# Kernel optimization log

Hardware: AMD Instinct MI355X
Metric: run time of the kernel (lower is better)

## Reference

```python
import math
import jax, jax.numpy as jnp
import numpy as np

B, T, D, H = 1, 4096, 1024, 16
HD = D // H  # 64

def setup_inputs() -> dict:
    key = jax.random.key(0)
    k1, k2, k3 = jax.random.split(key, 3)
    x = jax.random.normal(k1, (B, T, D), dtype=jnp.float32)
    # torch nn.Linear weight layout: [out_features, in_features]
    w_attn = jax.random.normal(k2, (3 * D, D), dtype=jnp.float32) * (1.0 / math.sqrt(D))
    w_proj = jax.random.normal(k3, (D, D), dtype=jnp.float32) * (1.0 / math.sqrt(D))
    return {"x": x, "w_attn": w_attn, "w_proj": w_proj}

def reference(x, w_attn, w_proj):
    b, t, d = x.shape
    qkv = jnp.einsum('btd,ed->bte', x, w_attn)  # [B,T,3D]
    q, k, v = jnp.split(qkv, 3, axis=-1)
    # [B,H,T,HD]
    q = q.reshape(b, t, H, HD).transpose(0, 2, 1, 3)
    k = k.reshape(b, t, H, HD).transpose(0, 2, 1, 3)
    v = v.reshape(b, t, H, HD).transpose(0, 2, 1, 3)
    scale = 1.0 / math.sqrt(HD)
    att = jnp.einsum('bhqd,bhkd->bhqk', q, k) * scale  # [B,H,T,T]
    causal = jnp.tril(jnp.ones((t, t), dtype=bool))
    att = jnp.where(causal[None, None], att, -jnp.inf)
    att = jax.nn.softmax(att, axis=-1)
    y = jnp.einsum('bhqk,bhkd->bhqd', att, v)  # [B,H,T,HD]
    y = y.transpose(0, 2, 1, 3).reshape(b, t, d)
    return jnp.einsum('btd,ed->bte', y, w_proj)
```

## Files before the change

### kernel.cpp

```cpp
#include <hip/hip_runtime.h>
#include <hip/hip_bf16.h>

typedef __bf16 bf16x8 __attribute__((ext_vector_type(8)));
typedef float  f32x4  __attribute__((ext_vector_type(4)));
typedef short  sh4    __attribute__((ext_vector_type(4)));

__device__ __forceinline__ void async_load16(const void* g, void* l) {
    __builtin_amdgcn_global_load_lds(
        (const __attribute__((address_space(1))) unsigned int*)g,
        (__attribute__((address_space(3))) unsigned int*)l,
        16, 0, 0);
}

__device__ __forceinline__ bool sniff_is_bf16(const void* src) {
    const unsigned int* p = (const unsigned int*)src;
    unsigned v = p[threadIdx.x & 63];
    unsigned e = (v >> 7) & 0xFF;
    unsigned long long m = __ballot(e >= 100 && e <= 140);
    return __popcll(m) >= 48;
}

__global__ __launch_bounds__(256) void to_bf16_3(
    const void* __restrict__ s0, const void* __restrict__ s1,
    const void* __restrict__ s2, __bf16* __restrict__ dst0) {
    const int b = blockIdx.x;
    const void* src; __bf16* dst; int boff;
    if (b < 4096)      { src = s0; dst = dst0;           boff = b; }
    else if (b < 7168) { src = s1; dst = dst0 + 4194304; boff = b - 4096; }
    else               { src = s2; dst = dst0 + 7340032; boff = b - 7168; }
    bool b16 = sniff_is_bf16(src);
    int i = boff * 1024 + threadIdx.x * 4;
    if (b16) {
        *(uint2*)(dst + i) = *(const uint2*)((const __bf16*)src + i);
    } else {
        float4 v = *(const float4*)((const float*)src + i);
        dst[i]     = (__bf16)v.x;
        dst[i + 1] = (__bf16)v.y;
        dst[i + 2] = (__bf16)v.z;
        dst[i + 3] = (__bf16)v.w;
    }
}

__global__ __launch_bounds__(256) void gemm_bt(
    const __bf16* __restrict__ A,
    const __bf16* __restrict__ B,
    __bf16* __restrict__ C,
    int M, int N, int K, int ldc,
    __bf16* __restrict__ vTout)
{
    __shared__ __bf16 As[3 * 128 * 32];
    __shared__ __bf16 Bs[3 * 128 * 32];

    const int nwg = gridDim.x;
    const int cpx = nwg >> 3;
    const int sid = (blockIdx.x & 7) * cpx + (blockIdx.x >> 3);
    const int nbx = N >> 7;
    const int bx  = sid % nbx;
    const int by  = sid / nbx;

    const int tid  = threadIdx.x;
    const int lane = tid & 63;
    const int w    = tid >> 6;
    const int wm   = w >> 1, wn = w & 1;
    const int m0   = by * 128;
    const int n0   = bx * 128;
    const int c    = lane & 15;
    const int g    = lane >> 4;

    f32x4 acc[4][4] = {};

    const int e0 = tid * 8;
    const int e1 = e0 + 2048;
    const int r0 = e0 >> 5, c0 = e0 & 31;
    const int r1 = e1 >> 5, c1 = e1 & 31;

    const __bf16* a0 = A + (size_t)(m0 + r0) * K + c0;
    const __bf16* a1 = A + (size_t)(m0 + r1) * K + c1;
    const __bf16* b0 = B + (size_t)(n0 + r0) * K + c0;
    const __bf16* b1 = B + (size_t)(n0 + r1) * K + c1;

    const int KT = K >> 5;

    async_load16(a0, As + e0);
    async_load16(a1, As + e1);
    async_load16(b0, Bs + e0);
    async_load16(b1, Bs + e1);
    async_load16(a0 + 32, As + 4096 + e0);
    async_load16(a1 + 32, As + 4096 + e1);
    async_load16(b0 + 32, Bs + 4096 + e0);
    async_load16(b1 + 32, Bs + 4096 + e1);

    int cb = 0, sb = 2;
    for (int kt = 0; kt < KT; ++kt) {
        if (kt + 1 < KT) asm volatile("s_waitcnt vmcnt(4)" ::: "memory");
        else             asm volatile("s_waitcnt vmcnt(0)" ::: "memory");
        __builtin_amdgcn_s_barrier();
        asm volatile("" ::: "memory");

        if (kt + 2 < KT) {
            const int k0 = (kt + 2) << 5;
            async_load16(a0 + k0, As + sb * 4096 + e0);
            async_load16(a1 + k0, As + sb * 4096 + e1);
            async_load16(b0 + k0, Bs + sb * 4096 + e0);
            async_load16(b1 + k0, Bs + sb * 4096 + e1);
        }

        const __bf16* as_ = As + cb * 4096;
        const __bf16* bs_ = Bs + cb * 4096;

        bf16x8 af[4], bfr[4];
        #pragma unroll
        for (int i = 0; i < 4; i++)
            af[i] = *(const bf16x8*)&as_[(wm * 64 + i * 16 + c) * 32 + g * 8];
        #pragma unroll
        for (int j = 0; j < 4; j++)
            bfr[j] = *(const bf16x8*)&bs_[(wn * 64 + j * 16 + c) * 32 + g * 8];
        #pragma unroll
        for (int i = 0; i < 4; i++)
            #pragma unroll
            for (int j = 0; j < 4; j++)
                acc[i][j] = __builtin_amdgcn_mfma_f32_16x16x32_bf16(af[i], bfr[j], acc[i][j], 0, 0, 0);

        cb = (cb == 2) ? 0 : cb + 1;
        sb = (sb == 2) ? 0 : sb + 1;
    }

    if (vTout && n0 >= ldc) {
        const int h0 = (n0 - ldc) >> 6;
        __bf16* Lt = As;
        __syncthreads();
        #pragma unroll
        for (int p = 0; p < 2; p++) {
            if (wn == p) {
                #pragma unroll
                for (int i = 0; i < 4; i++)
                    #pragma unroll
                    for (int j = 0; j < 4; j++) {
                        __bf16 tb[4] __attribute__((aligned(8)));
                        #pragma unroll
                        for (int r = 0; r < 4; r++) tb[r] = (__bf16)acc[i][j][r];
                        *(uint2*)&Lt[(j * 16 + c) * 136 + wm * 64 + i * 16 + g * 4]
                            = *(const uint2*)tb;
                    }
            }
            __syncthreads();
            {
                const int dl = tid >> 2, t0 = (tid & 3) * 32;
                __bf16* dst = vTout + (size_t)(h0 + p) * 262144 + (size_t)dl * 4096 + m0 + t0;
                #pragma unroll
                for (int k = 0; k < 4; k++)
                    *(bf16x8*)(dst + k * 8) = *(const bf16x8*)&Lt[dl * 136 + t0 + k * 8];
            }
            __syncthreads();
        }
        return;
    }

    #pragma unroll
    for (int i = 0; i < 4; i++) {
        const int row0 = m0 + wm * 64 + i * 16 + g * 4;
        #pragma unroll
        for (int j = 0; j < 4; j++) {
            const int col = n0 + wn * 64 + j * 16 + c;
            #pragma unroll
            for (int r = 0; r < 4; r++) {
                const size_t idx = (size_t)(row0 + r) * ldc + col;
                C[idx] = (__bf16)acc[i][j][r];
            }
        }
    }
}

__global__ __launch_bounds__(256) void gemm_bt64(
    const __bf16* __restrict__ A,
    const __bf16* __restrict__ B,
    void* __restrict__ Cv,
    int M, int N, int K,
    const void* sniff)
{
    bool out_b16 = true;
    if (sniff) out_b16 = sniff_is_bf16(sniff);

    __shared__ __bf16 As[3 * 128 * 32];
    __shared__ __bf16 Bs[3 * 64 * 32];

    const int nwg = gridDim.x;
    const int cpx = nwg >> 3;
    const int sid = (blockIdx.x & 7) * cpx + (blockIdx.x >> 3);
    const int nbx = N >> 6;
    const int bx  = sid % nbx;
    const int by  = sid / nbx;

    const int tid  = threadIdx.x;
    const int lane = tid & 63;
    const int w    = tid >> 6;
    const int wm   = w >> 1, wn = w & 1;
    const int m0   = by * 128;
    const int n0   = bx * 64;
    const int c    = lane & 15;
    const int g    = lane >> 4;

    f32x4 acc[4][2] = {};

    const int e0 = tid * 8;
    const int e1 = e0 + 2048;
    const int r0 = e0 >> 5, c0 = e0 & 31;
    const int r1 = e1 >> 5, c1 = e1 & 31;
    const int rb = tid >> 2, cbk = (tid & 3) * 8;

    const __bf16* a0 = A + (size_t)(m0 + r0) * K + c0;
    const __bf16* a1 = A + (size_t)(m0 + r1) * K + c1;
    const __bf16* bp = B + (size_t)(n0 + rb) * K + cbk;

    const int KT = K >> 5;

    async_load16(a0, As + e0);
    async_load16(a1, As + e1);
    async_load16(bp, Bs + e0);
    async_load16(a0 + 32, As + 4096 + e0);
    async_load16(a1 + 32, As + 4096 + e1);
    async_load16(bp + 32, Bs + 2048 + e0);

    int cb = 0, sb = 2;
    for (int kt = 0; kt < KT; ++kt) {
        if (kt + 1 < KT) asm volatile("s_waitcnt vmcnt(3)" ::: "memory");
        else             asm volatile("s_waitcnt vmcnt(0)" ::: "memory");
        __builtin_amdgcn_s_barrier();
        asm volatile("" ::: "memory");

        if (kt + 2 < KT) {
            const int k0 = (kt + 2) << 5;
            async_load16(a0 + k0, As + sb * 4096 + e0);
            async_load16(a1 + k0, As + sb * 4096 + e1);
            async_load16(bp + k0, Bs + sb * 2048 + e0);
        }

        const __bf16* as_ = As + cb * 4096;
        const __bf16* bs_ = Bs + cb * 2048;

        bf16x8 af[4], bfr[2];
        #pragma unroll
        for (int i = 0; i < 4; i++)
            af[i] = *(const bf16x8*)&as_[(wm * 64 + i * 16 + c) * 32 + g * 8];
        #pragma unroll
        for (int j = 0; j < 2; j++)
            bfr[j] = *(const bf16x8*)&bs_[(wn * 32 + j * 16 + c) * 32 + g * 8];
        #pragma unroll
        for (int i = 0; i < 4; i++)
            #pragma unroll
            for (int j = 0; j < 2; j++)
                acc[i][j] = __builtin_amdgcn_mfma_f32_16x16x32_bf16(af[i], bfr[j], acc[i][j], 0, 0, 0);

        cb = (cb == 2) ? 0 : cb + 1;
        sb = (sb == 2) ? 0 : sb + 1;
    }

    #pragma unroll
    for (int i = 0; i < 4; i++) {
        const int row0 = m0 + wm * 64 + i * 16 + g * 4;
        #pragma unroll
        for (int j = 0; j < 2; j++) {
            const int col = n0 + wn * 32 + j * 16 + c;
            #pragma unroll
            for (int r = 0; r < 4; r++) {
                const size_t idx = (size_t)(row0 + r) * N + col;
                if (out_b16) ((__bf16*)Cv)[idx] = (__bf16)acc[i][j][r];
                else         ((float*)Cv)[idx]  = acc[i][j][r];
            }
        }
    }
}

__global__ __launch_bounds__(512, 4) void attn_fwd(
    const __bf16* __restrict__ qkv,
    const __bf16* __restrict__ vT,
    __bf16* __restrict__ y)
{
    constexpr int LDQ = 2048;
    constexpr float SCL = 0.18033688011112042f;

    __shared__ __align__(16) char raw[50176];
    __bf16* ksb = (__bf16*)raw;
    __bf16* vsb = (__bf16*)(raw + 24576);
    float*  ls  = (float*)(raw + 49152);
    float*  F   = (float*)raw;

    const int id   = blockIdx.x;
    const int h    = (id & 7) * 2 + (id >> 8);
    const int pr   = (id >> 3) & 31;
    const int tid  = threadIdx.x;
    const int lane = tid & 63;
    const int w    = tid >> 6;
    const int kw   = w & 3;
    const int qw   = w >> 2;
    const int c    = lane & 15;
    const int g    = lane >> 4;
    const int qoff = h * 64;

    const int sr = tid >> 3, sg = ((tid & 7) ^ (sr & 7)) * 8;
    const __bf16* vbase = vT + (size_t)h * 262144;

    sh4 ones;
    #pragma unroll
    for (int i = 0; i < 4; i++) ones[i] = (short)0x3F80;

    const int qts[2] = {63 - pr, pr};

    #pragma unroll 1
    for (int ph = 0; ph < 2; ph++) {
        const int qt  = qts[ph];
        const int qs  = qt * 64;
        const int nkt = qt + 1;

        __syncthreads();

        async_load16(qkv + (size_t)sr * LDQ + 1024 + qoff + sg, ksb + tid * 8);
        async_load16(vbase + (size_t)sr * 4096 + sg, vsb + tid * 8);
        if (nkt > 1) {
            async_load16(qkv + (size_t)(64 + sr) * LDQ + 1024 + qoff + sg, ksb + 4096 + tid * 8);
            async_load16(vbase + (size_t)sr * 4096 + 64 + sg, vsb + 4096 + tid * 8);
        }

        bf16x8 qf[2][2];
        #pragma unroll
        for (int n = 0; n < 2; n++) {
            const __bf16* qrow = qkv + (size_t)(qs + qw * 32 + n * 16 + c) * LDQ + qoff;
            bf16x8 q0 = *(const bf16x8*)(qrow + g * 8);
            bf16x8 q1 = *(const bf16x8*)(qrow + 32 + g * 8);
            #pragma unroll
            for (int i = 0; i < 8; i++) {
                qf[n][0][i] = (__bf16)((float)q0[i] * SCL);
                qf[n][1][i] = (__bf16)((float)q1[i] * SCL);
            }
        }

        f32x4 ol[2] = {};
        f32x4 o[4][2] = {};

        for (int t = 0; t < nkt; t++) {
            if (t + 1 < nkt) asm volatile("s_waitcnt vmcnt(2)" ::: "memory");
            else             asm volatile("s_waitcnt vmcnt(0)" ::: "memory");
            __builtin_amdgcn_s_barrier();
            asm volatile("" ::: "memory");

            if (t + 2 < nkt) {
                const int nks = (t + 2) * 64;
                const int nb  = (t + 2) % 3;
                async_load16(qkv + (size_t)(nks + sr) * LDQ + 1024 + qoff + sg, ksb + (nb * 4096 + tid * 8));
                async_load16(vbase + (size_t)sr * 4096 + nks + sg, vsb + (nb * 4096 + tid * 8));
            }

            const __bf16* ks_ = ksb + (t % 3) * 4096;
            const __bf16* vs_ = vsb + (t % 3) * 4096;

            f32x4 sa[2] = {};
            #pragma unroll
            for (int s = 0; s < 2; s++) {
                bf16x8 kf = *(const bf16x8*)&ks_[(kw * 16 + c) * 64 + ((s * 4 + g) ^ (c & 7)) * 8];
                #pragma unroll
                for (int n = 0; n < 2; n++)
                    sa[n] = __builtin_amdgcn_mfma_f32_16x16x32_bf16(kf, qf[n][s], sa[n], 0, 0, 0);
            }

            if (t == nkt - 1) {
                #pragma unroll
                for (int n = 0; n < 2; n++)
                    #pragma unroll
                    for (int r = 0; r < 4; r++)
                        if (kw * 16 + g * 4 + r > qw * 32 + n * 16 + c) sa[n][r] = -1e30f;
            }

            sh4 vf[4];
            #pragma unroll
            for (int j = 0; j < 4; j++)
                vf[j] = *(const sh4*)&vs_[(j * 16 + c) * 64 + ((2 * kw + (g >> 1)) ^ (c & 7)) * 8 + (g & 1) * 4];

            #pragma unroll
            for (int n = 0; n < 2; n++) {
                __bf16 pb[4] __attribute__((aligned(8)));
                #pragma unroll
                for (int r = 0; r < 4; r++)
                    pb[r] = (__bf16)__builtin_amdgcn_exp2f(sa[n][r]);
                sh4 pbs = *(const sh4*)pb;
                ol[n] = __builtin_amdgcn_mfma_f32_16x16x16bf16_1k(ones, pbs, ol[n], 0, 0, 0);
                #pragma unroll
                for (int j = 0; j < 4; j++)
                    o[j][n] = __builtin_amdgcn_mfma_f32_16x16x16bf16_1k(vf[j], pbs, o[j][n], 0, 0, 0);
            }
        }

        __syncthreads();
        if (g == 0) {
            #pragma unroll
            for (int n = 0; n < 2; n++) ls[(kw * 4 + qw * 2 + n) * 16 + c] = ol[n][0];
        }
        __syncthreads();
        float rl = 0.f;
        if (w < 4) {
            float l_run = ls[(0 * 4 + w) * 16 + c] + ls[(1 * 4 + w) * 16 + c]
                        + ls[(2 * 4 + w) * 16 + c] + ls[(3 * 4 + w) * 16 + c];
            rl = 1.0f / l_run;
        }

        #pragma unroll
        for (int j = 0; j < 4; j++) {
            __syncthreads();
            #pragma unroll
            for (int n = 0; n < 2; n++)
                *(f32x4*)&F[((kw * 64) + (qw * 32 + n * 16 + c)) * 20 + g * 4] = o[j][n];
            __syncthreads();
            if (w < 4) {
                f32x4 t0 = *(const f32x4*)&F[((0 * 64) + (w * 16 + c)) * 20 + g * 4];
                f32x4 t1 = *(const f32x4*)&F[((1 * 64) + (w * 16 + c)) * 20 + g * 4];
                f32x4 t2 = *(const f32x4*)&F[((2 * 64) + (w * 16 + c)) * 20 + g * 4];
                f32x4 t3 = *(const f32x4*)&F[((3 * 64) + (w * 16 + c)) * 20 + g * 4];
                f32x4 tt = t0 + t1 + t2 + t3;
                __bf16 ob[4] __attribute__((aligned(8)));
                #pragma unroll
                for (int r = 0; r < 4; r++) ob[r] = (__bf16)(tt[r] * rl);
                *(uint2*)&y[(size_t)(qs + w * 16 + c) * 1024 + qoff + j * 16 + g * 4]
                    = *(const uint2*)ob;
            }
        }
    }
}

extern "C" void kernel_launch(void* const* d_in, const int* in_sizes, int n_in,
                              void* d_out, int out_size, void* d_ws, size_t ws_size,
                              hipStream_t stream) {
    constexpr int T = 4096, D = 1024;

    __bf16* cx   = (__bf16*)d_ws;
    __bf16* cwa  = cx  + (size_t)T * D;
    __bf16* cwp  = cwa + (size_t)3 * D * D;
    __bf16* qkv  = cwp + (size_t)D * D;
    __bf16* vT   = qkv + (size_t)T * 2048;
    __bf16* y    = vT  + (size_t)16 * 64 * T;

    to_bf16_3<<<8192, 256, 0, stream>>>(d_in[0], d_in[1], d_in[2], cx);
    gemm_bt<<<(3 * D / 128) * (T / 128), 256, 0, stream>>>(cx, cwa, qkv, T, 3 * D, D, 2048, vT);
    attn_fwd<<<512, 512, 0, stream>>>(qkv, vT, y);
    gemm_bt64<<<(D / 64) * (T / 128), 256, 0, stream>>>(y, cwp, d_out, T, D, D, d_in[2]);
}
```

Measured before the change: 190.1 us.

## Widen attention KV tile to 128 keys with double buffering

The attention kernel now processes 128 keys per iteration instead of 64. Each wave handles two 16-key sub-blocks, and the K/V LDS staging moves from a triple-buffered 64-key scheme to a double-buffered 128-key scheme. This halves the number of loop iterations and barriers and gives more MFMA work per sync. In exchange, LDS use rises to about 65KB, which may lower occupancy. Prefetch depth drops to one tile ahead and every iteration waits on vmcnt(0), so load latency may be less well hidden. The causal mask now works on absolute positions so it can handle a diagonal tile that falls partway through the 128-key tile.

Measured after the change: 192.3 us. About the same (+1.1%).

```diff
diff --git a/kernel.cpp b/kernel.cpp
--- a/kernel.cpp
+++ b/kernel.cpp
@@ -279,10 +279,10 @@
     constexpr int LDQ = 2048;
     constexpr float SCL = 0.18033688011112042f;
 
-    __shared__ __align__(16) char raw[50176];
+    __shared__ __align__(16) char raw[66560];
     __bf16* ksb = (__bf16*)raw;
-    __bf16* vsb = (__bf16*)(raw + 24576);
-    float*  ls  = (float*)(raw + 49152);
+    __bf16* vsb = (__bf16*)(raw + 32768);
+    float*  ls  = (float*)(raw + 65536);
     float*  F   = (float*)raw;
 
     const int id   = blockIdx.x;
@@ -297,7 +297,11 @@
     const int g    = lane >> 4;
     const int qoff = h * 64;
 
-    const int sr = tid >> 3, sg = ((tid & 7) ^ (sr & 7)) * 8;
+    const int p1  = tid + 512;
+    const int kr0 = tid >> 3, kc0 = ((tid & 7) ^ (kr0 & 7)) * 8;
+    const int kr1 = p1 >> 3,  kc1 = ((p1 & 7) ^ (kr1 & 7)) * 8;
+    const int dr0 = tid >> 4, vc0 = ((tid & 15) ^ (dr0 & 7)) * 8;
+    const int dr1 = p1 >> 4,  vc1 = ((p1 & 15) ^ (dr1 & 7)) * 8;
     const __bf16* vbase = vT + (size_t)h * 262144;
 
     sh4 ones;
@@ -310,16 +314,14 @@
     for (int ph = 0; ph < 2; ph++) {
         const int qt  = qts[ph];
         const int qs  = qt * 64;
-        const int nkt = qt + 1;
+        const int nkt = (qt >> 1) + 1;
 
         __syncthreads();
 
-        async_load16(qkv + (size_t)sr * LDQ + 1024 + qoff + sg, ksb + tid * 8);
-        async_load16(vbase + (size_t)sr * 4096 + sg, vsb + tid * 8);
-        if (nkt > 1) {
-            async_load16(qkv + (size_t)(64 + sr) * LDQ + 1024 + qoff + sg, ksb + 4096 + tid * 8);
-            async_load16(vbase + (size_t)sr * 4096 + 64 + sg, vsb + 4096 + tid * 8);
-        }
+        async_load16(qkv + (size_t)kr0 * LDQ + 1024 + qoff + kc0, ksb + tid * 8);
+        async_load16(qkv + (size_t)kr1 * LDQ + 1024 + qoff + kc1, ksb + p1 * 8);
+        async_load16(vbase + (size_t)dr0 * 4096 + vc0, vsb + tid * 8);
+        async_load16(vbase + (size_t)dr1 * 4096 + vc1, vsb + p1 * 8);
 
         bf16x8 qf[2][2];
         #pragma unroll
@@ -338,54 +340,66 @@
         f32x4 o[4][2] = {};
 
         for (int t = 0; t < nkt; t++) {
-            if (t + 1 < nkt) asm volatile("s_waitcnt vmcnt(2)" ::: "memory");
-            else             asm volatile("s_waitcnt vmcnt(0)" ::: "memory");
+            asm volatile("s_waitcnt vmcnt(0)" ::: "memory");
             __builtin_amdgcn_s_barrier();
             asm volatile("" ::: "memory");
 
-            if (t + 2 < nkt) {
-                const int nks = (t + 2) * 64;
-                const int nb  = (t + 2) % 3;
-                async_load16(qkv + (size_t)(nks + sr) * LDQ + 1024 + qoff + sg, ksb + (nb * 4096 + tid * 8));
-                async_load16(vbase + (size_t)sr * 4096 + nks + sg, vsb + (nb * 4096 + tid * 8));
-            }
-
-            const __bf16* ks_ = ksb + (t % 3) * 4096;
-            const __bf16* vs_ = vsb + (t % 3) * 4096;
-
-            f32x4 sa[2] = {};
+            if (t + 1 < nkt) {
+                const int nks = (t + 1) * 128;
+                const int nb  = (t + 1) & 1;
+                async_load16(qkv + (size_t)(nks + kr0) * LDQ + 1024 + qoff + kc0, ksb + (nb * 8192 + tid * 8));
+                async_load16(qkv + (size_t)(nks + kr1) * LDQ + 1024 + qoff + kc1, ksb + (nb * 8192 + p1 * 8));
+                async_load16(vbase + (size_t)dr0 * 4096 + nks + vc0, vsb + (nb * 8192 + tid * 8));
+                async_load16(vbase + (size_t)dr1 * 4096 + nks + vc1, vsb + (nb * 8192 + p1 * 8));
+            }
+
+            const __bf16* ks_ = ksb + (t & 1) * 8192;
+            const __bf16* vs_ = vsb + (t & 1) * 8192;
+
+            f32x4 sa[2][2] = {};
             #pragma unroll
             for (int s = 0; s < 2; s++) {
-                bf16x8 kf = *(const bf16x8*)&ks_[(kw * 16 + c) * 64 + ((s * 4 + g) ^ (c & 7)) * 8];
-                #pragma unroll
-                for (int n = 0; n < 2; n++)
-                    sa[n] = __builtin_amdgcn_mfma_f32_16x16x32_bf16(kf, qf[n][s], sa[n], 0, 0, 0);
+                #pragma unroll
+                for (int b = 0; b < 2; b++) {
+                    bf16x8 kf = *(const bf16x8*)&ks_[((2 * kw + b) * 16 + c) * 64 + ((s * 4 + g) ^ (c & 7)) * 8];
+                    #pragma unroll
+                    for (int n = 0; n < 2; n++)
+                        sa[b][n] = __builtin_amdgcn_mfma_f32_16x16x32_bf16(kf, qf[n][s], sa[b][n], 0, 0, 0);
+                }
             }
 
             if (t == nkt - 1) {
                 #pragma unroll
-                for (int n = 0; n < 2; n++)
+                for (int b = 0; b < 2; b++)
+                    #pragma unroll
+                    for (int n = 0; n < 2; n++)
+                        #pragma unroll
+                        for (int r = 0; r < 4; r++)
+                            if (t * 128 + (2 * kw + b) * 16 + g * 4 + r > qw * 32 + n * 16 + c + qs)
+                                sa[b][n][r] = -1e30f;
+            }
+
+            sh4 vf[2][4];
+            #pragma unroll
+            for (int b = 0; b < 2; b++)
+                #pragma unroll
+                for (int j = 0; j < 4; j++)
+                    vf[b][j] = *(const sh4*)&vs_[(j * 16 + c) * 128 + (((2 * kw + b) * 2 + (g >> 1)) ^ (c & 7)) * 8 + (g & 1) * 4];
+
+            #pragma unroll
+            for (int b = 0; b < 2; b++) {
+                #pragma unroll
+                for (int n = 0; n < 2; n++) {
+                    __bf16 pb[4] __attribute__((aligned(8)));
                     #pragma unroll
                     for (int r = 0; r < 4; r++)
-                        if (kw * 16 + g * 4 + r > qw * 32 + n * 16 + c) sa[n][r] = -1e30f;
-            }
-
-            sh4 vf[4];
-            #pragma unroll
-            for (int j = 0; j < 4; j++)
-                vf[j] = *(const sh4*)&vs_[(j * 16 + c) * 64 + ((2 * kw + (g >> 1)) ^ (c & 7)) * 8 + (g & 1) * 4];
-
-            #pragma unroll
-            for (int n = 0; n < 2; n++) {
-                __bf16 pb[4] __attribute__((aligned(8)));
-                #pragma unroll
-                for (int r = 0; r < 4; r++)
-                    pb[r] = (__bf16)__builtin_amdgcn_exp2f(sa[n][r]);
-                sh4 pbs = *(const sh4*)pb;
-                ol[n] = __builtin_amdgcn_mfma_f32_16x16x16bf16_1k(ones, pbs, ol[n], 0, 0, 0);
-                #pragma unroll
-                for (int j = 0; j < 4; j++)
-                    o[j][n] = __builtin_amdgcn_mfma_f32_16x16x16bf16_1k(vf[j], pbs, o[j][n], 0, 0, 0);
+                        pb[r] = (__bf16)__builtin_amdgcn_exp2f(sa[b][n][r]);
+                    sh4 pbs = *(const sh4*)pb;
+                    ol[n] = __builtin_amdgcn_mfma_f32_16x16x16bf16_1k(ones, pbs, ol[n], 0, 0, 0);
+                    #pragma unroll
+                    for (int j = 0; j < 4; j++)
+                        o[j][n] = __builtin_amdgcn_mfma_f32_16x16x16bf16_1k(vf[b][j], pbs, o[j][n], 0, 0, 0);
+                }
             }
         }
 
```
